# Kernel optimization log

Measured on AMD Instinct MI355X. Metric: run time of the kernel, lower is better.

Reference implementation:

```python
import jax, jax.numpy as jnp
import numpy as np
from jax import lax

KS = 3            # kernel_size
K = 32            # cluster_num
NB = 32           # num_base_kernels
HID = 64          # mlp_hidden_dim
COUT = 64         # out_channels
MAX_ITER = 20
TOL = 0.005


def _unfold3(x):
    # torch nn.Unfold(k=3, pad=1): output channel order is (c, kh, kw)
    b, c, h, w = x.shape
    xp = jnp.pad(x, ((0, 0), (0, 0), (1, 1), (1, 1)))
    cols = [xp[:, :, i:i + h, j:j + w] for i in range(KS) for j in range(KS)]
    p = jnp.stack(cols, axis=2)  # [B, C, 9, H, W]
    return p.reshape(b, c * KS * KS, h * w).transpose(0, 2, 1)  # [B, HW, C*9]


def _kmeans_single(key, sample):
    # sample: [N, D]. Lloyd iterations with early stop on total center shift.
    n, d = sample.shape
    centers0 = sample[jax.random.permutation(key, n)[:K]]

    def assign(centers):
        d2 = (jnp.sum(sample * sample, 1, keepdims=True)
              - 2.0 * (sample @ centers.T)
              + jnp.sum(centers * centers, 1))
        return jnp.argmin(d2, axis=1)

    def body(carry):
        i, centers, _ = carry
        a = assign(centers)
        oh = jax.nn.one_hot(a, K, dtype=sample.dtype)  # [N, K]
        counts = oh.sum(0)                             # [K]
        sums = oh.T @ sample                           # [K, D]
        new = jnp.where(counts[:, None] > 0,
                        sums / jnp.maximum(counts, 1.0)[:, None],
                        centers)
        shift = jnp.sum(jnp.linalg.norm(new - centers, axis=1))
        return (i + 1, new, shift)

    def cond(carry):
        i, _, shift = carry
        return jnp.logical_and(i < MAX_ITER, shift >= TOL * n)

    init = (jnp.int32(0), centers0, jnp.asarray(jnp.inf, sample.dtype))
    _, centers, _ = lax.while_loop(cond, body, init)
    return assign(centers)


def _kmeans(features):
    keys = jax.random.split(jax.random.key(42), features.shape[0])
    return jax.vmap(_kmeans_single)(keys, features)


def _mlp(x, w1, b1, w2, b2, w3, b3):
    h = jax.nn.relu(x @ w1 + b1)
    h = jax.nn.relu(h @ w2 + b2)
    return h @ w3 + b3


def setup_inputs() -> dict:
    key = jax.random.key(0)
    ks = jax.random.split(key, 16)
    B, C, H, W = 2, 32, 64, 64
    F = C * KS * KS
    fan = 1.0 / np.sqrt(F)
    fanh = 1.0 / np.sqrt(HID)
    return {
        'x': jax.random.normal(ks[0], (B, C, H, W), jnp.float32),
        'base_kernels': jax.random.normal(ks[1], (NB, F, COUT), jnp.float32) * np.sqrt(2.0 / F),
        'kg_w1': jax.random.normal(ks[2], (F, HID), jnp.float32) * fan,
        'kg_b1': jnp.zeros((HID,), jnp.float32),
        'kg_w2': jax.random.normal(ks[3], (HID, HID), jnp.float32) * fanh,
        'kg_b2': jnp.zeros((HID,), jnp.float32),
        'kg_w3': jax.random.normal(ks[4], (HID, NB), jnp.float32) * fanh,
        'kg_b3': jnp.zeros((NB,), jnp.float32),
        'bg_w1': jax.random.normal(ks[5], (F, HID), jnp.float32) * fan,
        'bg_b1': jnp.zeros((HID,), jnp.float32),
        'bg_w2': jax.random.normal(ks[6], (HID, HID), jnp.float32) * fanh,
        'bg_b2': jnp.zeros((HID,), jnp.float32),
        'bg_w3': jax.random.normal(ks[7], (HID, COUT), jnp.float32) * fanh,
        'bg_b3': jnp.zeros((COUT,), jnp.float32),
    }


def reference(x, base_kernels, kg_w1, kg_b1, kg_w2, kg_b2, kg_w3, kg_b3,
              bg_w1, bg_b1, bg_w2, bg_b2, bg_w3, bg_b3):
    B, C, H, W = x.shape
    patches = _unfold3(x)  # [B, P, F] with F = C*9
    P = patches.shape[1]
    # observation features: mean over kernel area per channel
    obs = patches.reshape(B, P, C, KS * KS).mean(-1)  # [B, P, C]
    idx = _kmeans(obs)  # [B, P] int cluster assignments

    # per-cluster centers of the full patch features (scatter-mean)
    oh = jax.nn.one_hot(idx, K, dtype=patches.dtype)          # [B, P, K]
    sums = jnp.einsum('bpk,bpf->bkf', oh, patches)            # [B, K, F]
    counts = jnp.maximum(oh.sum(1), 1.0)                      # [B, K]
    centers = sums / counts[:, :, None]                       # [B, K, F]

    # adaptive kernels = softmax-mixture of base kernels
    attn = jax.nn.softmax(_mlp(centers, kg_w1, kg_b1, kg_w2, kg_b2, kg_w3, kg_b3), axis=-1)  # [B,K,NB]
    kernels = jnp.einsum('bkn,nfc->bkfc', attn, base_kernels)  # [B, K, F, COUT]
    biases = _mlp(centers, bg_w1, bg_b1, bg_w2, bg_b2, bg_w3, bg_b3)  # [B, K, COUT]

    # combine: out[b,p] = patches[b,p] @ kernels[b, idx[b,p]] + biases[b, idx[b,p]]
    bidx = jnp.arange(B)[:, None]
    wtok = kernels[bidx, idx]   # [B, P, F, COUT]
    btok = biases[bidx, idx]    # [B, P, COUT]
    out = jnp.einsum('bpf,bpfc->bpc', patches, wtok) + btok
    out = out.transpose(0, 2, 1).reshape(B, COUT, H, W)
    return (out, idx)
```

## Files before the change

### kernel.cpp

```cpp
#include <hip/hip_runtime.h>
#include <hip/hip_bf16.h>
#include <vector>
#include <algorithm>
#include <utility>
#include <stdint.h>

#define BB 2
#define PP 4096
#define FF 288
#define KK 32
#define NBASE 32
#define HID 64
#define COUT 64
#define NWG_KM 32
#define SUBS 16
#define OUT_ELEMS 524288

#define THREEFRY_PARTITIONABLE 1

typedef unsigned short u16;

#define OFF_IDX    512
#define OFF_ATTN   33280
#define OFF_BIAS   41472
#define OFF_PART   57856
#define OFF_CNTS   320000
#define OFF_CPART  328192
#define OFF_WG     1544704
#define OFF_BAR2   3904000
#define OFF_CSAVE  3906048

struct InitIdx { int v[2][32]; };

__device__ __forceinline__ float bf2f(u16 u){
  union { unsigned int i; float f; } cv; cv.i = ((unsigned int)u) << 16; return cv.f;
}
__device__ __forceinline__ u16 f2bf(float f){
  union { float f; unsigned int i; } cv; cv.f = f;
  unsigned int x = cv.i;
  unsigned int r = (x + 0x7FFFu + ((x >> 16) & 1u)) >> 16;
  return (u16)r;
}
__device__ __forceinline__ float u_lo(unsigned int u){
  union { unsigned int i; float f; } cv; cv.i = u << 16; return cv.f;
}
__device__ __forceinline__ float u_hi(unsigned int u){
  union { unsigned int i; float f; } cv; cv.i = u & 0xFFFF0000u; return cv.f;
}

__device__ __forceinline__ void st_agent(float* p, float v){
  __hip_atomic_store(reinterpret_cast<unsigned int*>(p), __float_as_uint(v),
                     __ATOMIC_RELAXED, __HIP_MEMORY_SCOPE_AGENT);
}
__device__ __forceinline__ float ld_agent(const float* p){
  unsigned int u = __hip_atomic_load(reinterpret_cast<const unsigned int*>(p),
                                     __ATOMIC_RELAXED, __HIP_MEMORY_SCOPE_AGENT);
  return __uint_as_float(u);
}
__device__ __forceinline__ void st_slot(int* p, int v){
  __hip_atomic_store(p, v, __ATOMIC_RELAXED, __HIP_MEMORY_SCOPE_AGENT);
}
__device__ __forceinline__ int ld_slot(const int* p){
  return __hip_atomic_load(p, __ATOMIC_RELAXED, __HIP_MEMORY_SCOPE_AGENT);
}

template<bool BF>
__device__ __forceinline__ float ld(const void* p, size_t i){
  if constexpr (BF) { return bf2f(((const u16*)p)[i]); }
  else              { return ((const float*)p)[i]; }
}
template<bool BF>
__device__ __forceinline__ void st(void* p, size_t i, float v){
  if constexpr (BF) { ((u16*)p)[i] = f2bf(v); }
  else              { ((float*)p)[i] = v; }
}

__device__ __forceinline__ bool self_detect(const void* x, int* cntS){
  const int t = threadIdx.x, nb = blockDim.x;
  if (t == 0) *cntS = 0;
  __syncthreads();
  const u16* p = (const u16*)x;
  int bad = 0;
  for (int i = t; i < 1024; i += nb){
    u16 u = p[2*i];
    unsigned e = (u >> 7) & 0xFFu;
    if (e >= 131u) ++bad;
  }
  if (bad) atomicAdd(cntS, bad);
  __syncthreads();
  bool r = (*cntS < 102);
  __syncthreads();
  return r;
}

template<bool BF>
__device__ __forceinline__ float obs_chan(const void* x, size_t bi, int h, int w){
  float s = 0.f;
  #pragma unroll
  for (int dh=-1; dh<=1; ++dh){
    int hh = h + dh;
    #pragma unroll
    for (int dw=-1; dw<=1; ++dw){
      int ww = w + dw;
      float v = 0.f;
      if ((unsigned)hh < 64u && (unsigned)ww < 64u) v = ld<BF>(x, bi + (hh<<6) + ww);
      s += v;
    }
  }
  return s / 9.0f;
}

__device__ __forceinline__ void gbar16(int* slots, int mb, int sub, int epoch){
  asm volatile("s_waitcnt vmcnt(0)" ::: "memory");
  __syncthreads();
  const int t = threadIdx.x;
  if (t == 0) st_slot(&slots[(mb*16 + sub)*16], epoch);
  if (t < 16){
    while (ld_slot(&slots[(mb*16 + t)*16]) < epoch){}
  }
  __atomic_signal_fence(__ATOMIC_SEQ_CST);
  __syncthreads();
}

template<bool BF, bool FIRST>
__device__ void kB_body(const void* __restrict__ x,
                        float* __restrict__ part,
                        float* __restrict__ cnts,
                        int* __restrict__ idxg,
                        void* __restrict__ dout,
                        int* __restrict__ slots,
                        float* __restrict__ centSave,
                        int* __restrict__ actSave,
                        const InitIdx& ii,
                        float* obs_st, float* cent, float* cc_s, int* a_loc,
                        float* sq, float* snorm, float* cntsh,
                        float* acc8, float* cnt8){
  const int t   = threadIdx.x;
  const int wg  = blockIdx.x;
  const int mb  = wg >> 4;
  const int sub = wg & 15;
  const int pg  = sub*256 + t;
  const int d   = t & 31, oct = t >> 5;

  float o[32];
  {
    int h = pg >> 6, w = pg & 63;
    size_t xb = (size_t)mb << 17;
    for (int c=0; c<32; ++c){
      float v = obs_chan<BF>(x, xb + ((size_t)c<<12), h, w);
      o[c] = v; obs_st[t*33 + c] = v;
    }
  }
  bool act;
  if constexpr (FIRST){
    if (t < 32){
      int q = ii.v[mb][t];
      int qh = q >> 6, qw = q & 63;
      size_t xq = (size_t)mb << 17;
      for (int c=0; c<32; ++c) cent[t*32 + c] = obs_chan<BF>(x, xq + ((size_t)c<<12), qh, qw);
    }
    act = true;
  } else {
    for (int e=t; e<1024; e+=256) cent[e] = centSave[mb*1024 + e];
    act = (actSave[mb] != 0);
  }
  __syncthreads();

  float ss = 0.f;
  #pragma unroll
  for (int dd=0; dd<32; ++dd) ss = fmaf(o[dd], o[dd], ss);

  int parity = 0;
  const int itBeg = FIRST ? 0 : 10;
  const int itEnd = FIRST ? 10 : 20;

  for (int it=itBeg; it<itEnd && act; ++it){
    if (t < 32){
      float s = 0.f;
      #pragma unroll
      for (int dd=0; dd<32; ++dd){ float v = cent[t*32 + dd]; s = fmaf(v,v,s); }
      cc_s[t] = s;
    }
    __syncthreads();
    float best = 3.0e38f; int bk = 0;
    for (int k=0; k<32; k+=4){
      const float4* c0 = (const float4*)&cent[(k  )*32];
      const float4* c1 = (const float4*)&cent[(k+1)*32];
      const float4* c2 = (const float4*)&cent[(k+2)*32];
      const float4* c3 = (const float4*)&cent[(k+3)*32];
      float dt0=0.f, dt1=0.f, dt2=0.f, dt3=0.f;
      #pragma unroll
      for (int q=0; q<8; ++q){
        float4 a0 = c0[q], a1 = c1[q], a2 = c2[q], a3 = c3[q];
        float o0 = o[q*4+0], o1 = o[q*4+1], o2 = o[q*4+2], o3 = o[q*4+3];
        dt0 = fmaf(o0,a0.x,dt0); dt0 = fmaf(o1,a0.y,dt0); dt0 = fmaf(o2,a0.z,dt0); dt0 = fmaf(o3,a0.w,dt0);
        dt1 = fmaf(o0,a1.x,dt1); dt1 = fmaf(o1,a1.y,dt1); dt1 = fmaf(o2,a1.z,dt1); dt1 = fmaf(o3,a1.w,dt1);
        dt2 = fmaf(o0,a2.x,dt2); dt2 = fmaf(o1,a2.y,dt2); dt2 = fmaf(o2,a2.z,dt2); dt2 = fmaf(o3,a2.w,dt2);
        dt3 = fmaf(o0,a3.x,dt3); dt3 = fmaf(o1,a3.y,dt3); dt3 = fmaf(o2,a3.z,dt3); dt3 = fmaf(o3,a3.w,dt3);
      }
      float di0 = (ss - 2.0f*dt0) + cc_s[k];
      float di1 = (ss - 2.0f*dt1) + cc_s[k+1];
      float di2 = (ss - 2.0f*dt2) + cc_s[k+2];
      float di3 = (ss - 2.0f*dt3) + cc_s[k+3];
      if (di0 < best){ best = di0; bk = k; }
      if (di1 < best){ best = di1; bk = k+1; }
      if (di2 < best){ best = di2; bk = k+2; }
      if (di3 < best){ best = di3; bk = k+3; }
    }
    a_loc[t] = bk;
    __syncthreads();
    for (int e=t; e<8*32*33; e+=256) acc8[e] = 0.f;
    cnt8[t] = 0.f;
    __syncthreads();
    {
      const int p0 = oct*32;
      int kcur = a_loc[p0];
      float racc = 0.f; int rl = 0;
      for (int i=0; i<32; ++i){
        int kp = a_loc[p0+i];
        float v = obs_st[(p0+i)*33 + d];
        if (kp != kcur){
          acc8[(oct*32 + kcur)*33 + d] += racc;
          if (d == 0) cnt8[oct*32 + kcur] += (float)rl;
          racc = 0.f; rl = 0; kcur = kp;
        }
        racc += v; ++rl;
      }
      acc8[(oct*32 + kcur)*33 + d] += racc;
      if (d == 0) cnt8[oct*32 + kcur] += (float)rl;
    }
    __syncthreads();
    float* Pg = part + ((size_t)((parity*2 + mb)*SUBS + sub))*1024;
    {
      float r0=0.f, r1=0.f, r2=0.f, r3=0.f;
      #pragma unroll
      for (int o2=0; o2<8; ++o2){
        r0 += acc8[(o2*32 + oct      )*33 + d];
        r1 += acc8[(o2*32 + oct + 8  )*33 + d];
        r2 += acc8[(o2*32 + oct + 16 )*33 + d];
        r3 += acc8[(o2*32 + oct + 24 )*33 + d];
      }
      st_agent(&Pg[(oct     )*32 + d], r0);
      st_agent(&Pg[(oct + 8 )*32 + d], r1);
      st_agent(&Pg[(oct + 16)*32 + d], r2);
      st_agent(&Pg[(oct + 24)*32 + d], r3);
    }
    if (t < 32){
      float c = 0.f;
      #pragma unroll
      for (int o2=0; o2<8; ++o2) c += cnt8[o2*32 + t];
      st_agent(&cnts[((size_t)((parity*2 + mb)*SUBS + sub))*32 + t], c);
    }
    gbar16(slots, mb, sub, it+1);
    {
      const float* Pb = part + (size_t)((parity*2 + mb)*SUBS)*1024;
      const float* Cb = cnts + (size_t)((parity*2 + mb)*SUBS)*32;
      if (t < 32){
        float s = 0.f;
        #pragma unroll
        for (int si=0; si<SUBS; ++si) s += ld_agent(&Cb[si*32 + t]);
        cntsh[t] = s;
      }
      __syncthreads();
      {
        int k = t >> 3, d4 = (t & 7) * 4;
        float vx = 0.f, vy = 0.f, vz = 0.f, vw = 0.f;
        #pragma unroll
        for (int si=0; si<SUBS; ++si){
          const float* pp = &Pb[si*1024 + k*32 + d4];
          float a0 = ld_agent(pp+0);
          float a1 = ld_agent(pp+1);
          float a2 = ld_agent(pp+2);
          float a3 = ld_agent(pp+3);
          vx += a0; vy += a1; vz += a2; vw += a3;
        }
        float cn = cntsh[k];
        float den = fmaxf(cn, 1.f);
        bool pos = cn > 0.f;
        float o0 = cent[k*32 + d4+0], o1 = cent[k*32 + d4+1];
        float o2 = cent[k*32 + d4+2], o3 = cent[k*32 + d4+3];
        float n0 = pos ? (vx / den) : o0;
        float n1 = pos ? (vy / den) : o1;
        float n2 = pos ? (vz / den) : o2;
        float n3 = pos ? (vw / den) : o3;
        float e0 = n0-o0, e1 = n1-o1, e2 = n2-o2, e3 = n3-o3;
        sq[k*32 + d4+0] = e0*e0; sq[k*32 + d4+1] = e1*e1;
        sq[k*32 + d4+2] = e2*e2; sq[k*32 + d4+3] = e3*e3;
        cent[k*32 + d4+0] = n0; cent[k*32 + d4+1] = n1;
        cent[k*32 + d4+2] = n2; cent[k*32 + d4+3] = n3;
      }
      __syncthreads();
      if (t < 32){
        float s = 0.f;
        #pragma unroll
        for (int dd=0; dd<32; ++dd) s += sq[t*32 + dd];
        snorm[t] = sqrtf(s);
      }
      __syncthreads();
      float sh = 0.f;
      for (int k=0;k<32;++k) sh += snorm[k];
      act = ((it+1) < 20) && ((double)sh >= 20.48);
      __syncthreads();
    }
    parity ^= 1;
  }

  if constexpr (FIRST){
    __syncthreads();
    if (sub == 0){
      for (int e=t; e<1024; e+=256) centSave[mb*1024 + e] = cent[e];
      if (t == 0) actSave[mb] = act ? 1 : 0;
    }
    return;
  } else {
    if (t == 0) st_slot(&slots[(mb*16 + sub)*16], 0x7FFFFFFF);
    __syncthreads();
    if (t < 32){
      float s = 0.f;
      #pragma unroll
      for (int dd=0; dd<32; ++dd){ float v = cent[t*32 + dd]; s = fmaf(v,v,s); }
      cc_s[t] = s;
    }
    __syncthreads();
    float best = 3.0e38f; int bk = 0;
    for (int k=0; k<32; k+=4){
      const float4* c0 = (const float4*)&cent[(k  )*32];
      const float4* c1 = (const float4*)&cent[(k+1)*32];
      const float4* c2 = (const float4*)&cent[(k+2)*32];
      const float4* c3 = (const float4*)&cent[(k+3)*32];
      float dt0=0.f, dt1=0.f, dt2=0.f, dt3=0.f;
      #pragma unroll
      for (int q=0; q<8; ++q){
        float4 a0 = c0[q], a1 = c1[q], a2 = c2[q], a3 = c3[q];
        float o0 = o[q*4+0], o1 = o[q*4+1], o2 = o[q*4+2], o3 = o[q*4+3];
        dt0 = fmaf(o0,a0.x,dt0); dt0 = fmaf(o1,a0.y,dt0); dt0 = fmaf(o2,a0.z,dt0); dt0 = fmaf(o3,a0.w,dt0);
        dt1 = fmaf(o0,a1.x,dt1); dt1 = fmaf(o1,a1.y,dt1); dt1 = fmaf(o2,a1.z,dt1); dt1 = fmaf(o3,a1.w,dt1);
        dt2 = fmaf(o0,a2.x,dt2); dt2 = fmaf(o1,a2.y,dt2); dt2 = fmaf(o2,a2.z,dt2); dt2 = fmaf(o3,a2.w,dt2);
        dt3 = fmaf(o0,a3.x,dt3); dt3 = fmaf(o1,a3.y,dt3); dt3 = fmaf(o2,a3.z,dt3); dt3 = fmaf(o3,a3.w,dt3);
      }
      float di0 = (ss - 2.0f*dt0) + cc_s[k];
      float di1 = (ss - 2.0f*dt1) + cc_s[k+1];
      float di2 = (ss - 2.0f*dt2) + cc_s[k+2];
      float di3 = (ss - 2.0f*dt3) + cc_s[k+3];
      if (di0 < best){ best = di0; bk = k; }
      if (di1 < best){ best = di1; bk = k+1; }
      if (di2 < best){ best = di2; bk = k+2; }
      if (di3 < best){ best = di3; bk = k+3; }
    }
    idxg[mb*PP + pg] = bk;
    st<BF>(dout, (size_t)OUT_ELEMS + mb*PP + pg, (float)bk);
  }
}

template<bool FIRST>
__global__ __launch_bounds__(256) void kBsplit(const void* x, float* part, float* cnts,
                                               int* idxg, void* dout,
                                               int* slots, float* centSave, int* actSave,
                                               InitIdx ii){
  __shared__ __align__(16) float obs_st[256*33];
  __shared__ __align__(16) float cent[32*32];
  __shared__ float cc_s[32];
  __shared__ int   a_loc[256];
  __shared__ float sq[32*32];
  __shared__ float snorm[32];
  __shared__ float cntsh[32];
  __shared__ float acc8[8*32*33];
  __shared__ float cnt8[8*32];
  __shared__ int   cntS;
  if (self_detect(x, &cntS))
       kB_body<true , FIRST>(x, part, cnts, idxg, dout, slots, centSave, actSave, ii,
                             obs_st, cent, cc_s, a_loc, sq, snorm, cntsh, acc8, cnt8);
  else kB_body<false, FIRST>(x, part, cnts, idxg, dout, slots, centSave, actSave, ii,
                             obs_st, cent, cc_s, a_loc, sq, snorm, cntsh, acc8, cnt8);
}

template<bool BF>
__device__ void kC_body(const void* __restrict__ x,
                        const int* __restrict__ idxg,
                        float* __restrict__ cpartJ,
                        float* __restrict__ tv,
                        int* __restrict__ idxsh,
                        float* __restrict__ acc8,
                        float* __restrict__ cnt8){
  int wgid = blockIdx.x;
  int cg = wgid / 9, j = wgid % 9;
  int b = cg >> 4, pc = cg & 15;
  int t = threadIdx.x;
  const int d = t & 31, oct = t >> 5;

  idxsh[t] = idxg[b*PP + pc*256 + t];
  int dh = j/3 - 1, dw = j%3 - 1;
  for (int e=t; e<8192; e+=256){
    int c = e >> 8, p = e & 255;
    int gp = (pc << 8) + p;
    int h = gp >> 6, w = gp & 63;
    int hh = h + dh, ww = w + dw;
    float v = 0.f;
    if ((unsigned)hh < 64u && (unsigned)ww < 64u)
      v = ld<BF>(x, ((size_t)b << 17) + ((size_t)c << 12) + (hh<<6) + ww);
    tv[p*33 + c] = v;
  }
  for (int e=t; e<8*32*33; e+=256) acc8[e] = 0.f;
  cnt8[t] = 0.f;
  __syncthreads();
  {
    const int p0 = oct*32;
    int kcur = idxsh[p0];
    float racc = 0.f; int rl = 0;
    for (int i=0; i<32; ++i){
      int kp = idxsh[p0+i];
      float v = tv[(p0+i)*33 + d];
      if (kp != kcur){
        acc8[(oct*32 + kcur)*33 + d] += racc;
        if (d == 0) cnt8[oct*32 + kcur] += (float)rl;
        racc = 0.f; rl = 0; kcur = kp;
      }
      racc += v; ++rl;
    }
    acc8[(oct*32 + kcur)*33 + d] += racc;
    if (d == 0) cnt8[oct*32 + kcur] += (float)rl;
  }
  __syncthreads();
  float* cp = cpartJ + (size_t)wgid*(32*33);
  {
    float r0=0.f, r1=0.f, r2=0.f, r3=0.f;
    #pragma unroll
    for (int o2=0; o2<8; ++o2){
      r0 += acc8[(o2*32 + oct      )*33 + d];
      r1 += acc8[(o2*32 + oct + 8  )*33 + d];
      r2 += acc8[(o2*32 + oct + 16 )*33 + d];
      r3 += acc8[(o2*32 + oct + 24 )*33 + d];
    }
    cp[(oct     )*33 + d] = r0;
    cp[(oct + 8 )*33 + d] = r1;
    cp[(oct + 16)*33 + d] = r2;
    cp[(oct + 24)*33 + d] = r3;
  }
  if (j == 0 && t < 32){
    float c8 = 0.f;
    #pragma unroll
    for (int o2=0; o2<8; ++o2) c8 += cnt8[o2*32 + t];
    cp[t*33 + 32] = c8;
  }
}

__global__ __launch_bounds__(256) void kC(const void* x, const int* idxg,
                                          float* cpartJ){
  __shared__ __align__(16) float tv[256*33];
  __shared__ int   idxsh[256];
  __shared__ __align__(16) float acc8[8*32*33];
  __shared__ float cnt8[256];
  __shared__ int   cntS;
  if (self_detect(x, &cntS)) kC_body<true >(x, idxg, cpartJ, tv, idxsh, acc8, cnt8);
  else                       kC_body<false>(x, idxg, cpartJ, tv, idxsh, acc8, cnt8);
}

template<bool BF>
__device__ void kD_body(const float* __restrict__ cpartJ,
                        const void* kg_w1, const void* kg_b1,
                        const void* kg_w2, const void* kg_b2,
                        const void* kg_w3, const void* kg_b3,
                        const void* bg_w1, const void* bg_b1,
                        const void* bg_w2, const void* bg_b2,
                        const void* bg_w3, const void* bg_b3,
                        float* __restrict__ attn,
                        float* __restrict__ biasO,
                        float* __restrict__ row,
                        float* __restrict__ h1,
                        float* __restrict__ h2,
                        float* __restrict__ lgs){
  int wg = blockIdx.x; int b = wg >> 5; int k = wg & 31;
  int t = threadIdx.x;
  float cnt = 0.f;
  for (int ch=0; ch<16; ++ch)
    cnt += cpartJ[(size_t)((b*16+ch)*9)*(32*33) + k*33 + 32];
  float den = fmaxf(cnt, 1.f);
  for (int f=t; f<FF; f+=64){
    int c = f / 9, j = f % 9;
    float s = 0.f;
    for (int ch=0; ch<16; ++ch)
      s += cpartJ[(size_t)((b*16+ch)*9 + j)*(32*33) + k*33 + c];
    row[f] = s / den;
  }
  __syncthreads();

  {
    float s = 0.f;
    #pragma unroll 8
    for (int f=0; f<FF; ++f) s = fmaf(row[f], ld<BF>(kg_w1, f*HID + t), s);
    h1[t] = fmaxf(s + ld<BF>(kg_b1, t), 0.f);
  }
  __syncthreads();
  {
    float s = 0.f;
    #pragma unroll 8
    for (int h=0; h<HID; ++h) s = fmaf(h1[h], ld<BF>(kg_w2, h*HID + t), s);
    h2[t] = fmaxf(s + ld<BF>(kg_b2, t), 0.f);
  }
  __syncthreads();
  if (t < 32){
    float s = 0.f;
    #pragma unroll 8
    for (int h=0; h<HID; ++h) s = fmaf(h2[h], ld<BF>(kg_w3, h*NBASE + t), s);
    lgs[t] = s + ld<BF>(kg_b3, t);
  }
  __syncthreads();
  if (t < 32){
    float mx = -3.0e38f;
    for (int i=0;i<NBASE;++i) mx = fmaxf(mx, lgs[i]);
    float se = 0.f;
    for (int i=0;i<NBASE;++i) se += expf(lgs[i]-mx);
    attn[wg*NBASE + t] = expf(lgs[t]-mx) / se;
  }
  __syncthreads();
  {
    float s = 0.f;
    #pragma unroll 8
    for (int f=0; f<FF; ++f) s = fmaf(row[f], ld<BF>(bg_w1, f*HID + t), s);
    h1[t] = fmaxf(s + ld<BF>(bg_b1, t), 0.f);
  }
  __syncthreads();
  {
    float s = 0.f;
    #pragma unroll 8
    for (int h=0; h<HID; ++h) s = fmaf(h1[h], ld<BF>(bg_w2, h*HID + t), s);
    h2[t] = fmaxf(s + ld<BF>(bg_b2, t), 0.f);
  }
  __syncthreads();
  {
    float s = 0.f;
    #pragma unroll 8
    for (int h=0; h<HID; ++h) s = fmaf(h1[h] * 0.f + h2[h], ld<BF>(bg_w3, h*COUT + t), s);
    biasO[wg*COUT + t] = s + ld<BF>(bg_b3, t);
  }
}

__global__ __launch_bounds__(64) void kD(const void* x, const float* cpartJ,
                                         const void* kg_w1, const void* kg_b1,
                                         const void* kg_w2, const void* kg_b2,
                                         const void* kg_w3, const void* kg_b3,
                                         const void* bg_w1, const void* bg_b1,
                                         const void* bg_w2, const void* bg_b2,
                                         const void* bg_w3, const void* bg_b3,
                                         float* attn, float* biasO){
  __shared__ float row[FF];
  __shared__ float h1[64];
  __shared__ float h2[64];
  __shared__ float lgs[32];
  __shared__ int   cntS;
  if (self_detect(x, &cntS))
       kD_body<true >(cpartJ, kg_w1,kg_b1,kg_w2,kg_b2,kg_w3,kg_b3,
                      bg_w1,bg_b1,bg_w2,bg_b2,bg_w3,bg_b3, attn, biasO, row,h1,h2,lgs);
  else kD_body<false>(cpartJ, kg_w1,kg_b1,kg_w2,kg_b2,kg_w3,kg_b3,
                      bg_w1,bg_b1,bg_w2,bg_b2,bg_w3,bg_b3, attn, biasO, row,h1,h2,lgs);
}

template<bool BF>
__device__ void kE_body(const void* __restrict__ base,
                        const float* __restrict__ attn,
                        u16* __restrict__ Wg,
                        float* __restrict__ at,
                        float* __restrict__ tile){
  int wg = blockIdx.x;
  int fq = wg & 3, bk = wg >> 2;
  int t = threadIdx.x;
  if (t < 32) at[t] = attn[bk*NBASE + t];
  __syncthreads();
  int f0 = fq*72;
  for (int e8 = t; e8 < 72*8; e8 += 256){
    int fl = e8 >> 3, cg = (e8 & 7) << 3;
    float s0=0.f,s1=0.f,s2=0.f,s3=0.f,s4=0.f,s5=0.f,s6=0.f,s7=0.f;
    if constexpr (BF){
      const u16* bp = (const u16*)base + (size_t)(f0 + fl)*COUT + cg;
      #pragma unroll 4
      for (int n=0; n<NBASE; ++n){
        uint4 v = *(const uint4*)(bp + (size_t)n*FF*COUT);
        float a = at[n];
        s0 = fmaf(a, u_lo(v.x), s0); s1 = fmaf(a, u_hi(v.x), s1);
        s2 = fmaf(a, u_lo(v.y), s2); s3 = fmaf(a, u_hi(v.y), s3);
        s4 = fmaf(a, u_lo(v.z), s4); s5 = fmaf(a, u_hi(v.z), s5);
        s6 = fmaf(a, u_lo(v.w), s6); s7 = fmaf(a, u_hi(v.w), s7);
      }
    } else {
      const float* bp = (const float*)base + (size_t)(f0 + fl)*COUT + cg;
      #pragma unroll 4
      for (int n=0; n<NBASE; ++n){
        float4 v0 = *(const float4*)(bp + (size_t)n*FF*COUT);
        float4 v1 = *(const float4*)(bp + (size_t)n*FF*COUT + 4);
        float a = at[n];
        s0 = fmaf(a, v0.x, s0); s1 = fmaf(a, v0.y, s1);
        s2 = fmaf(a, v0.z, s2); s3 = fmaf(a, v0.w, s3);
        s4 = fmaf(a, v1.x, s4); s5 = fmaf(a, v1.y, s5);
        s6 = fmaf(a, v1.z, s6); s7 = fmaf(a, v1.w, s7);
      }
    }
    float* tp = &tile[fl*65 + cg];
    tp[0]=s0; tp[1]=s1; tp[2]=s2; tp[3]=s3;
    tp[4]=s4; tp[5]=s5; tp[6]=s6; tp[7]=s7;
  }
  __syncthreads();
  for (int e=t; e<72*64; e+=256){
    int c = e / 72, fl = e % 72;
    Wg[(size_t)bk*(64*FF) + (size_t)c*FF + f0 + fl] = f2bf(tile[fl*65 + c]);
  }
}

__global__ __launch_bounds__(256) void kE(const void* x, const void* base,
                                          const float* attn, u16* Wg){
  __shared__ float at[32];
  __shared__ float tile[72*65];
  __shared__ int   cntS;
  if (self_detect(x, &cntS)) kE_body<true >(base, attn, Wg, at, tile);
  else                       kE_body<false>(base, attn, Wg, at, tile);
}

template<bool BF>
__device__ void kF_body(const void* __restrict__ x,
                        const int* __restrict__ idxg,
                        const u16* __restrict__ Wg,
                        const float* __restrict__ biasO,
                        void* __restrict__ dout,
                        u16* __restrict__ patch,
                        float* __restrict__ outT){
  int wg = blockIdx.x;
  int q = wg & 3, h = (wg >> 2) & 63, b = wg >> 8;
  int t = threadIdx.x, wv = t >> 6, lane = t & 63;
  int w0 = q << 4;

  for (int e=t; e<16*FF; e+=256){
    int pl = e & 15, fe = e >> 4;
    int c = fe / 9, j = fe % 9;
    int hh = h + j/3 - 1, ww = w0 + pl + (j%3) - 1;
    float v = 0.f;
    if ((unsigned)hh < 64u && (unsigned)ww < 64u)
      v = ld<BF>(x, ((size_t)b << 17) + ((size_t)c << 12) + (hh<<6) + ww);
    patch[pl*296 + fe] = f2bf(v);
  }
  __syncthreads();

  #pragma unroll
  for (int i=0; i<4; ++i){
    int pl = (wv << 2) + i;
    int p = (h << 6) + w0 + pl;
    int k = idxg[(b << 12) + p];
    const uint4* Wp = (const uint4*)(Wg + ((size_t)((b << 5) + k)*64 + lane)*FF);
    const uint4* Pp = (const uint4*)(patch + pl*296);
    float acc = 0.f;
    #pragma unroll 6
    for (int j=0; j<36; ++j){
      uint4 wv4 = Wp[j];
      uint4 pv4 = Pp[j];
      acc = fmaf(u_lo(pv4.x), u_lo(wv4.x), acc);
      acc = fmaf(u_hi(pv4.x), u_hi(wv4.x), acc);
      acc = fmaf(u_lo(pv4.y), u_lo(wv4.y), acc);
      acc = fmaf(u_hi(pv4.y), u_hi(wv4.y), acc);
      acc = fmaf(u_lo(pv4.z), u_lo(wv4.z), acc);
      acc = fmaf(u_hi(pv4.z), u_hi(wv4.z), acc);
      acc = fmaf(u_lo(pv4.w), u_lo(wv4.w), acc);
      acc = fmaf(u_hi(pv4.w), u_hi(wv4.w), acc);
    }
    float bias = biasO[((b << 5) + k)*COUT + lane];
    outT[lane*17 + pl] = acc + bias;
  }
  __syncthreads();

  for (int e=t; e<1024; e+=256){
    int cout = e >> 4, pl = e & 15;
    st<BF>(dout, (((size_t)(b << 6) + cout) << 12) + (h << 6) + w0 + pl,
           outT[cout*17 + pl]);
  }
}

__global__ __launch_bounds__(256) void kF(const void* x, const int* idxg,
                                          const u16* Wg, const float* biasO,
                                          void* dout){
  __shared__ u16   patch[16*296];
  __shared__ float outT[64*17];
  __shared__ int   cntS;
  if (self_detect(x, &cntS)) kF_body<true >(x, idxg, Wg, biasO, dout, patch, outT);
  else                       kF_body<false>(x, idxg, Wg, biasO, dout, patch, outT);
}

static inline uint32_t rotl32(uint32_t x, int d){ return (x<<d)|(x>>(32-d)); }
static void tf_block(uint32_t k0,uint32_t k1,uint32_t x0,uint32_t x1,uint32_t&o0,uint32_t&o1){
  uint32_t ks2 = k0 ^ k1 ^ 0x1BD11BDAu;
  uint32_t v0 = x0 + k0, v1 = x1 + k1;
  const int ra[4]={13,15,26,6}, rb[4]={17,29,16,24};
  #define R4(r) for(int i_=0;i_<4;++i_){ v0 += v1; v1 = rotl32(v1,(r)[i_]); v1 ^= v0; }
  R4(ra); v0 += k1;  v1 += ks2 + 1u;
  R4(rb); v0 += ks2; v1 += k0  + 2u;
  R4(ra); v0 += k0;  v1 += k1  + 3u;
  R4(rb); v0 += k1;  v1 += ks2 + 4u;
  R4(ra); v0 += ks2; v1 += k0  + 5u;
  #undef R4
  o0 = v0; o1 = v1;
}
struct KP{ uint32_t a, b; };
static void tf_split(KP k, KP& first, KP& second){
#if THREEFRY_PARTITIONABLE
  uint32_t a0,b0,a1,b1;
  tf_block(k.a,k.b, 0u,0u, a0,b0);
  tf_block(k.a,k.b, 0u,1u, a1,b1);
  first  = KP{a0,b0};
  second = KP{a1,b1};
#else
  uint32_t a0,b0,a1,b1;
  tf_block(k.a,k.b, 0u,2u, a0,b0);
  tf_block(k.a,k.b, 1u,3u, a1,b1);
  first  = KP{a0,a1};
  second = KP{b0,b1};
#endif
}
static void random_bits_4096(KP k, std::vector<uint32_t>& bits){
#if THREEFRY_PARTITIONABLE
  for (int i=0;i<4096;++i){
    uint32_t o0,o1; tf_block(k.a,k.b, 0u,(uint32_t)i, o0,o1);
    bits[i] = o0 ^ o1;
  }
#else
  for (int i=0;i<2048;++i){
    uint32_t o0,o1; tf_block(k.a,k.b,(uint32_t)i,(uint32_t)(i+2048),o0,o1);
    bits[i] = o0; bits[i+2048] = o1;
  }
#endif
}
static void perm_first32(KP key, int* out32){
  std::vector<int> vals(4096);
  for (int i=0;i<4096;++i) vals[i] = i;
  std::vector<uint32_t> bits(4096);
  std::vector<std::pair<uint32_t,int>> pr(4096);
  KP k = key;
  for (int r=0;r<2;++r){
    KP nk, sk; tf_split(k, nk, sk); k = nk;
    random_bits_4096(sk, bits);
    for (int i=0;i<4096;++i) pr[i] = std::make_pair(bits[i], vals[i]);
    std::stable_sort(pr.begin(), pr.end(),
        [](const std::pair<uint32_t,int>& a, const std::pair<uint32_t,int>& c){ return a.first < c.first; });
    for (int i=0;i<4096;++i) vals[i] = pr[i].second;
  }
  for (int j=0;j<32;++j) out32[j] = vals[j];
}

extern "C" void kernel_launch(void* const* d_in, const int* in_sizes, int n_in,
                              void* d_out, int out_size, void* d_ws, size_t ws_size,
                              hipStream_t stream) {
  const void* x     = d_in[0];
  const void* base  = d_in[1];
  const void* kg_w1 = d_in[2];
  const void* kg_b1 = d_in[3];
  const void* kg_w2 = d_in[4];
  const void* kg_b2 = d_in[5];
  const void* kg_w3 = d_in[6];
  const void* kg_b3 = d_in[7];
  const void* bg_w1 = d_in[8];
  const void* bg_b1 = d_in[9];
  const void* bg_w2 = d_in[10];
  const void* bg_b2 = d_in[11];
  const void* bg_w3 = d_in[12];
  const void* bg_b3 = d_in[13];

  char* ws = (char*)d_ws;
  int*   idxg  = (int*)(ws + OFF_IDX);
  float* attn  = (float*)(ws + OFF_ATTN);
  float* biasO = (float*)(ws + OFF_BIAS);
  float* part  = (float*)(ws + OFF_PART);
  float* cnts  = (float*)(ws + OFF_CNTS);
  float* cpartJ= (float*)(ws + OFF_CPART);
  u16*   Wg    = (u16*)(ws + OFF_WG);
  int*   slots = (int*)(ws + OFF_BAR2);
  float* centSave = (float*)(ws + OFF_CSAVE);
  int*   actSave  = slots + 8;

  InitIdx ii;
  KP root = KP{0u, 42u};
  KP kb0, kb1; tf_split(root, kb0, kb1);
  perm_first32(kb0, ii.v[0]);
  perm_first32(kb1, ii.v[1]);

  hipMemsetAsync(ws + OFF_BAR2, 0, 2048, stream);
  kBsplit<true ><<<NWG_KM, 256, 0, stream>>>(x, part, cnts, idxg, d_out, slots, centSave, actSave, ii);
  kBsplit<false><<<NWG_KM, 256, 0, stream>>>(x, part, cnts, idxg, d_out, slots, centSave, actSave, ii);
  kC<<<288, 256, 0, stream>>>(x, idxg, cpartJ);
  kD<<<64, 64, 0, stream>>>(x, cpartJ,
                            kg_w1, kg_b1, kg_w2, kg_b2, kg_w3, kg_b3,
                            bg_w1, bg_b1, bg_w2, bg_b2, bg_w3, bg_b3,
                            attn, biasO);
  kE<<<256, 256, 0, stream>>>(x, base, attn, Wg);
  kF<<<512, 256, 0, stream>>>(x, idxg, Wg, biasO, d_out);
}
```

Before: 289.6 us.

## Merge split k-means launches and fuse MLP with kernel-mixing stage

The two-launch k-means, which saved centroids and the active flag to workspace between halves, becomes a single kernel that runs all 20 iterations. The MLP kernel (kD) and the base-kernel mixing kernel (kE) are fused into one kDE launch, where each of the four f-quarter blocks recomputes the per-cluster MLP redundantly. The host-side threefry permutation is also computed once and cached in a static. The aim is to cut launch gaps and intermediate round trips, at the cost of about fourfold redundant MLP work across blocks.

```diff
diff --git a/kernel.cpp b/kernel.cpp
--- a/kernel.cpp
+++ b/kernel.cpp
@@ -21,14 +21,12 @@
 typedef unsigned short u16;
 
 #define OFF_IDX    512
-#define OFF_ATTN   33280
 #define OFF_BIAS   41472
 #define OFF_PART   57856
 #define OFF_CNTS   320000
 #define OFF_CPART  328192
 #define OFF_WG     1544704
 #define OFF_BAR2   3904000
-#define OFF_CSAVE  3906048
 
 struct InitIdx { int v[2][32]; };
 
@@ -122,15 +120,13 @@
   __syncthreads();
 }
 
-template<bool BF, bool FIRST>
+template<bool BF>
 __device__ void kB_body(const void* __restrict__ x,
                         float* __restrict__ part,
                         float* __restrict__ cnts,
                         int* __restrict__ idxg,
                         void* __restrict__ dout,
                         int* __restrict__ slots,
-                        float* __restrict__ centSave,
-                        int* __restrict__ actSave,
                         const InitIdx& ii,
                         float* obs_st, float* cent, float* cc_s, int* a_loc,
                         float* sq, float* snorm, float* cntsh,
@@ -151,18 +147,11 @@
       o[c] = v; obs_st[t*33 + c] = v;
     }
   }
-  bool act;
-  if constexpr (FIRST){
-    if (t < 32){
-      int q = ii.v[mb][t];
-      int qh = q >> 6, qw = q & 63;
-      size_t xq = (size_t)mb << 17;
-      for (int c=0; c<32; ++c) cent[t*32 + c] = obs_chan<BF>(x, xq + ((size_t)c<<12), qh, qw);
-    }
-    act = true;
-  } else {
-    for (int e=t; e<1024; e+=256) cent[e] = centSave[mb*1024 + e];
-    act = (actSave[mb] != 0);
+  if (t < 32){
+    int q = ii.v[mb][t];
+    int qh = q >> 6, qw = q & 63;
+    size_t xq = (size_t)mb << 17;
+    for (int c=0; c<32; ++c) cent[t*32 + c] = obs_chan<BF>(x, xq + ((size_t)c<<12), qh, qw);
   }
   __syncthreads();
 
@@ -170,11 +159,10 @@
   #pragma unroll
   for (int dd=0; dd<32; ++dd) ss = fmaf(o[dd], o[dd], ss);
 
+  bool act = true;
   int parity = 0;
-  const int itBeg = FIRST ? 0 : 10;
-  const int itEnd = FIRST ? 10 : 20;
-
-  for (int it=itBeg; it<itEnd && act; ++it){
+
+  for (int it=0; it<20 && act; ++it){
     if (t < 32){
       float s = 0.f;
       #pragma unroll
@@ -304,59 +292,47 @@
     }
     parity ^= 1;
   }
-
-  if constexpr (FIRST){
-    __syncthreads();
-    if (sub == 0){
-      for (int e=t; e<1024; e+=256) centSave[mb*1024 + e] = cent[e];
-      if (t == 0) actSave[mb] = act ? 1 : 0;
-    }
-    return;
-  } else {
-    if (t == 0) st_slot(&slots[(mb*16 + sub)*16], 0x7FFFFFFF);
-    __syncthreads();
-    if (t < 32){
-      float s = 0.f;
-      #pragma unroll
-      for (int dd=0; dd<32; ++dd){ float v = cent[t*32 + dd]; s = fmaf(v,v,s); }
-      cc_s[t] = s;
-    }
-    __syncthreads();
-    float best = 3.0e38f; int bk = 0;
-    for (int k=0; k<32; k+=4){
-      const float4* c0 = (const float4*)&cent[(k  )*32];
-      const float4* c1 = (const float4*)&cent[(k+1)*32];
-      const float4* c2 = (const float4*)&cent[(k+2)*32];
-      const float4* c3 = (const float4*)&cent[(k+3)*32];
-      float dt0=0.f, dt1=0.f, dt2=0.f, dt3=0.f;
-      #pragma unroll
-      for (int q=0; q<8; ++q){
-        float4 a0 = c0[q], a1 = c1[q], a2 = c2[q], a3 = c3[q];
-        float o0 = o[q*4+0], o1 = o[q*4+1], o2 = o[q*4+2], o3 = o[q*4+3];
-        dt0 = fmaf(o0,a0.x,dt0); dt0 = fmaf(o1,a0.y,dt0); dt0 = fmaf(o2,a0.z,dt0); dt0 = fmaf(o3,a0.w,dt0);
-        dt1 = fmaf(o0,a1.x,dt1); dt1 = fmaf(o1,a1.y,dt1); dt1 = fmaf(o2,a1.z,dt1); dt1 = fmaf(o3,a1.w,dt1);
-        dt2 = fmaf(o0,a2.x,dt2); dt2 = fmaf(o1,a2.y,dt2); dt2 = fmaf(o2,a2.z,dt2); dt2 = fmaf(o3,a2.w,dt2);
-        dt3 = fmaf(o0,a3.x,dt3); dt3 = fmaf(o1,a3.y,dt3); dt3 = fmaf(o2,a3.z,dt3); dt3 = fmaf(o3,a3.w,dt3);
-      }
-      float di0 = (ss - 2.0f*dt0) + cc_s[k];
-      float di1 = (ss - 2.0f*dt1) + cc_s[k+1];
-      float di2 = (ss - 2.0f*dt2) + cc_s[k+2];
-      float di3 = (ss - 2.0f*dt3) + cc_s[k+3];
-      if (di0 < best){ best = di0; bk = k; }
-      if (di1 < best){ best = di1; bk = k+1; }
-      if (di2 < best){ best = di2; bk = k+2; }
-      if (di3 < best){ best = di3; bk = k+3; }
-    }
-    idxg[mb*PP + pg] = bk;
-    st<BF>(dout, (size_t)OUT_ELEMS + mb*PP + pg, (float)bk);
-  }
-}
-
-template<bool FIRST>
-__global__ __launch_bounds__(256) void kBsplit(const void* x, float* part, float* cnts,
-                                               int* idxg, void* dout,
-                                               int* slots, float* centSave, int* actSave,
-                                               InitIdx ii){
+  if (t == 0) st_slot(&slots[(mb*16 + sub)*16], 0x7FFFFFFF);
+  __syncthreads();
+  if (t < 32){
+    float s = 0.f;
+    #pragma unroll
+    for (int dd=0; dd<32; ++dd){ float v = cent[t*32 + dd]; s = fmaf(v,v,s); }
+    cc_s[t] = s;
+  }
+  __syncthreads();
+  float best = 3.0e38f; int bk = 0;
+  for (int k=0; k<32; k+=4){
+    const float4* c0 = (const float4*)&cent[(k  )*32];
+    const float4* c1 = (const float4*)&cent[(k+1)*32];
+    const float4* c2 = (const float4*)&cent[(k+2)*32];
+    const float4* c3 = (const float4*)&cent[(k+3)*32];
+    float dt0=0.f, dt1=0.f, dt2=0.f, dt3=0.f;
+    #pragma unroll
+    for (int q=0; q<8; ++q){
+      float4 a0 = c0[q], a1 = c1[q], a2 = c2[q], a3 = c3[q];
+      float o0 = o[q*4+0], o1 = o[q*4+1], o2 = o[q*4+2], o3 = o[q*4+3];
+      dt0 = fmaf(o0,a0.x,dt0); dt0 = fmaf(o1,a0.y,dt0); dt0 = fmaf(o2,a0.z,dt0); dt0 = fmaf(o3,a0.w,dt0);
+      dt1 = fmaf(o0,a1.x,dt1); dt1 = fmaf(o1,a1.y,dt1); dt1 = fmaf(o2,a1.z,dt1); dt1 = fmaf(o3,a1.w,dt1);
+      dt2 = fmaf(o0,a2.x,dt2); dt2 = fmaf(o1,a2.y,dt2); dt2 = fmaf(o2,a2.z,dt2); dt2 = fmaf(o3,a2.w,dt2);
+      dt3 = fmaf(o0,a3.x,dt3); dt3 = fmaf(o1,a3.y,dt3); dt3 = fmaf(o2,a3.z,dt3); dt3 = fmaf(o3,a3.w,dt3);
+    }
+    float di0 = (ss - 2.0f*dt0) + cc_s[k];
+    float di1 = (ss - 2.0f*dt1) + cc_s[k+1];
+    float di2 = (ss - 2.0f*dt2) + cc_s[k+2];
+    float di3 = (ss - 2.0f*dt3) + cc_s[k+3];
+    if (di0 < best){ best = di0; bk = k; }
+    if (di1 < best){ best = di1; bk = k+1; }
+    if (di2 < best){ best = di2; bk = k+2; }
+    if (di3 < best){ best = di3; bk = k+3; }
+  }
+  idxg[mb*PP + pg] = bk;
+  st<BF>(dout, (size_t)OUT_ELEMS + mb*PP + pg, (float)bk);
+}
+
+__global__ __launch_bounds__(256) void kB(const void* x, float* part, float* cnts,
+                                          int* idxg, void* dout,
+                                          int* slots, InitIdx ii){
   __shared__ __align__(16) float obs_st[256*33];
   __shared__ __align__(16) float cent[32*32];
   __shared__ float cc_s[32];
@@ -368,10 +344,10 @@
   __shared__ float cnt8[8*32];
   __shared__ int   cntS;
   if (self_detect(x, &cntS))
-       kB_body<true , FIRST>(x, part, cnts, idxg, dout, slots, centSave, actSave, ii,
-                             obs_st, cent, cc_s, a_loc, sq, snorm, cntsh, acc8, cnt8);
-  else kB_body<false, FIRST>(x, part, cnts, idxg, dout, slots, centSave, actSave, ii,
-                             obs_st, cent, cc_s, a_loc, sq, snorm, cntsh, acc8, cnt8);
+       kB_body<true >(x, part, cnts, idxg, dout, slots, ii,
+                      obs_st, cent, cc_s, a_loc, sq, snorm, cntsh, acc8, cnt8);
+  else kB_body<false>(x, part, cnts, idxg, dout, slots, ii,
+                      obs_st, cent, cc_s, a_loc, sq, snorm, cntsh, acc8, cnt8);
 }
 
 template<bool BF>
@@ -456,42 +432,45 @@
 }
 
 template<bool BF>
-__device__ void kD_body(const float* __restrict__ cpartJ,
-                        const void* kg_w1, const void* kg_b1,
-                        const void* kg_w2, const void* kg_b2,
-                        const void* kg_w3, const void* kg_b3,
-                        const void* bg_w1, const void* bg_b1,
-                        const void* bg_w2, const void* bg_b2,
-                        const void* bg_w3, const void* bg_b3,
-                        float* __restrict__ attn,
-                        float* __restrict__ biasO,
-                        float* __restrict__ row,
-                        float* __restrict__ h1,
-                        float* __restrict__ h2,
-                        float* __restrict__ lgs){
-  int wg = blockIdx.x; int b = wg >> 5; int k = wg & 31;
+__device__ void kDE_body(const void* __restrict__ base,
+                         const float* __restrict__ cpartJ,
+                         const void* kg_w1, const void* kg_b1,
+                         const void* kg_w2, const void* kg_b2,
+                         const void* kg_w3, const void* kg_b3,
+                         const void* bg_w1, const void* bg_b1,
+                         const void* bg_w2, const void* bg_b2,
+                         const void* bg_w3, const void* bg_b3,
+                         float* __restrict__ biasO,
+                         u16* __restrict__ Wg,
+                         float* row, float* h1, float* h2, float* lgs,
+                         float* at, float* tile){
+  int wg = blockIdx.x;
+  int fq = wg & 3, bk = wg >> 2;
+  int b = bk >> 5, k = bk & 31;
   int t = threadIdx.x;
-  float cnt = 0.f;
-  for (int ch=0; ch<16; ++ch)
-    cnt += cpartJ[(size_t)((b*16+ch)*9)*(32*33) + k*33 + 32];
-  float den = fmaxf(cnt, 1.f);
-  for (int f=t; f<FF; f+=64){
-    int c = f / 9, j = f % 9;
-    float s = 0.f;
+
+  if (t < 64){
+    float cnt = 0.f;
     for (int ch=0; ch<16; ++ch)
-      s += cpartJ[(size_t)((b*16+ch)*9 + j)*(32*33) + k*33 + c];
-    row[f] = s / den;
-  }
-  __syncthreads();
-
-  {
+      cnt += cpartJ[(size_t)((b*16+ch)*9)*(32*33) + k*33 + 32];
+    float den = fmaxf(cnt, 1.f);
+    for (int f=t; f<FF; f+=64){
+      int c = f / 9, j = f % 9;
+      float s = 0.f;
+      for (int ch=0; ch<16; ++ch)
+        s += cpartJ[(size_t)((b*16+ch)*9 + j)*(32*33) + k*33 + c];
+      row[f] = s / den;
+    }
+  }
+  __syncthreads();
+  if (t < 64){
     float s = 0.f;
     #pragma unroll 8
     for (int f=0; f<FF; ++f) s = fmaf(row[f], ld<BF>(kg_w1, f*HID + t), s);
     h1[t] = fmaxf(s + ld<BF>(kg_b1, t), 0.f);
   }
   __syncthreads();
-  {
+  if (t < 64){
     float s = 0.f;
     #pragma unroll 8
     for (int h=0; h<HID; ++h) s = fmaf(h1[h], ld<BF>(kg_w2, h*HID + t), s);
@@ -510,62 +489,31 @@
     for (int i=0;i<NBASE;++i) mx = fmaxf(mx, lgs[i]);
     float se = 0.f;
     for (int i=0;i<NBASE;++i) se += expf(lgs[i]-mx);
-    attn[wg*NBASE + t] = expf(lgs[t]-mx) / se;
-  }
-  __syncthreads();
-  {
+    at[t] = expf(lgs[t]-mx) / se;
+  }
+  __syncthreads();
+  if (t < 64){
     float s = 0.f;
     #pragma unroll 8
     for (int f=0; f<FF; ++f) s = fmaf(row[f], ld<BF>(bg_w1, f*HID + t), s);
     h1[t] = fmaxf(s + ld<BF>(bg_b1, t), 0.f);
   }
   __syncthreads();
-  {
+  if (t < 64){
     float s = 0.f;
     #pragma unroll 8
     for (int h=0; h<HID; ++h) s = fmaf(h1[h], ld<BF>(bg_w2, h*HID + t), s);
     h2[t] = fmaxf(s + ld<BF>(bg_b2, t), 0.f);
   }
   __syncthreads();
-  {
+  if (t < 64 && fq == 0){
     float s = 0.f;
     #pragma unroll 8
-    for (int h=0; h<HID; ++h) s = fmaf(h1[h] * 0.f + h2[h], ld<BF>(bg_w3, h*COUT + t), s);
-    biasO[wg*COUT + t] = s + ld<BF>(bg_b3, t);
-  }
-}
-
-__global__ __launch_bounds__(64) void kD(const void* x, const float* cpartJ,
-                                         const void* kg_w1, const void* kg_b1,
-                                         const void* kg_w2, const void* kg_b2,
-                                         const void* kg_w3, const void* kg_b3,
-                                         const void* bg_w1, const void* bg_b1,
-                                         const void* bg_w2, const void* bg_b2,
-                                         const void* bg_w3, const void* bg_b3,
-                                         float* attn, float* biasO){
-  __shared__ float row[FF];
-  __shared__ float h1[64];
-  __shared__ float h2[64];
-  __shared__ float lgs[32];
-  __shared__ int   cntS;
-  if (self_detect(x, &cntS))
-       kD_body<true >(cpartJ, kg_w1,kg_b1,kg_w2,kg_b2,kg_w3,kg_b3,
-                      bg_w1,bg_b1,bg_w2,bg_b2,bg_w3,bg_b3, attn, biasO, row,h1,h2,lgs);
-  else kD_body<false>(cpartJ, kg_w1,kg_b1,kg_w2,kg_b2,kg_w3,kg_b3,
-                      bg_w1,bg_b1,bg_w2,bg_b2,bg_w3,bg_b3, attn, biasO, row,h1,h2,lgs);
-}
-
-template<bool BF>
-__device__ void kE_body(const void* __restrict__ base,
-                        const float* __restrict__ attn,
-                        u16* __restrict__ Wg,
-                        float* __restrict__ at,
-                        float* __restrict__ tile){
-  int wg = blockIdx.x;
-  int fq = wg & 3, bk = wg >> 2;
-  int t = threadIdx.x;
-  if (t < 32) at[t] = attn[bk*NBASE + t];
-  __syncthreads();
+    for (int h=0; h<HID; ++h) s = fmaf(h2[h], ld<BF>(bg_w3, h*COUT + t), s);
+    biasO[bk*COUT + t] = s + ld<BF>(bg_b3, t);
+  }
+  __syncthreads();
+
   int f0 = fq*72;
   for (int e8 = t; e8 < 72*8; e8 += 256){
     int fl = e8 >> 3, cg = (e8 & 7) << 3;
@@ -605,13 +553,29 @@
   }
 }
 
-__global__ __launch_bounds__(256) void kE(const void* x, const void* base,
-                                          const float* attn, u16* Wg){
+__global__ __launch_bounds__(256) void kDE(const void* x, const void* base,
+                         const float* cpartJ,
+                         const void* kg_w1, const void* kg_b1,
+                         const void* kg_w2, const void* kg_b2,
+                         const void* kg_w3, const void* kg_b3,
+                         const void* bg_w1, const void* bg_b1,
+                         const void* bg_w2, const void* bg_b2,
+                         const void* bg_w3, const void* bg_b3,
+                         float* biasO, u16* Wg){
+  __shared__ float row[FF];
+  __shared__ float h1[64];
+  __shared__ float h2[64];
+  __shared__ float lgs[32];
   __shared__ float at[32];
   __shared__ float tile[72*65];
   __shared__ int   cntS;
-  if (self_detect(x, &cntS)) kE_body<true >(base, attn, Wg, at, tile);
-  else                       kE_body<false>(base, attn, Wg, at, tile);
+  if (self_detect(x, &cntS))
+       kDE_body<true >(base, cpartJ, kg_w1,kg_b1,kg_w2,kg_b2,kg_w3,kg_b3,
+                       bg_w1,bg_b1,bg_w2,bg_b2,bg_w3,bg_b3, biasO, Wg,
+                       row,h1,h2,lgs,at,tile);
+  else kDE_body<false>(base, cpartJ, kg_w1,kg_b1,kg_w2,kg_b2,kg_w3,kg_b3,
+                       bg_w1,bg_b1,bg_w2,bg_b2,bg_w3,bg_b3, biasO, Wg,
+                       row,h1,h2,lgs,at,tile);
 }
 
 template<bool BF>
@@ -741,6 +705,18 @@
   for (int j=0;j<32;++j) out32[j] = vals[j];
 }
 
+static const InitIdx& get_init_idx(){
+  static const InitIdx ii = [](){
+    InitIdx r;
+    KP root = KP{0u, 42u};
+    KP kb0, kb1; tf_split(root, kb0, kb1);
+    perm_first32(kb0, r.v[0]);
+    perm_first32(kb1, r.v[1]);
+    return r;
+  }();
+  return ii;
+}
+
 extern "C" void kernel_launch(void* const* d_in, const int* in_sizes, int n_in,
                               void* d_out, int out_size, void* d_ws, size_t ws_size,
                               hipStream_t stream) {
@@ -761,30 +737,21 @@
 
   char* ws = (char*)d_ws;
   int*   idxg  = (int*)(ws + OFF_IDX);
-  float* attn  = (float*)(ws + OFF_ATTN);
   float* biasO = (float*)(ws + OFF_BIAS);
   float* part  = (float*)(ws + OFF_PART);
   float* cnts  = (float*)(ws + OFF_CNTS);
   float* cpartJ= (float*)(ws + OFF_CPART);
   u16*   Wg    = (u16*)(ws + OFF_WG);
   int*   slots = (int*)(ws + OFF_BAR2);
-  float* centSave = (float*)(ws + OFF_CSAVE);
-  int*   actSave  = slots + 8;
-
-  InitIdx ii;
-  KP root = KP{0u, 42u};
-  KP kb0, kb1; tf_split(root, kb0, kb1);
-  perm_first32(kb0, ii.v[0]);
-  perm_first32(kb1, ii.v[1]);
+
+  const InitIdx& ii = get_init_idx();
 
   hipMemsetAsync(ws + OFF_BAR2, 0, 2048, stream);
-  kBsplit<true ><<<NWG_KM, 256, 0, stream>>>(x, part, cnts, idxg, d_out, slots, centSave, actSave, ii);
-  kBsplit<false><<<NWG_KM, 256, 0, stream>>>(x, part, cnts, idxg, d_out, slots, centSave, actSave, ii);
+  kB<<<NWG_KM, 256, 0, stream>>>(x, part, cnts, idxg, d_out, slots, ii);
   kC<<<288, 256, 0, stream>>>(x, idxg, cpartJ);
-  kD<<<64, 64, 0, stream>>>(x, cpartJ,
-                            kg_w1, kg_b1, kg_w2, kg_b2, kg_w3, kg_b3,
-                            bg_w1, bg_b1, bg_w2, bg_b2, bg_w3, bg_b3,
-                            attn, biasO);
-  kE<<<256, 256, 0, stream>>>(x, base, attn, Wg);
+  kDE<<<256, 256, 0, stream>>>(x, base, cpartJ,
+                               kg_w1, kg_b1, kg_w2, kg_b2, kg_w3, kg_b3,
+                               bg_w1, bg_b1, bg_w2, bg_b2, bg_w3, bg_b3,
+                               biasO, Wg);
   kF<<<512, 256, 0, stream>>>(x, idxg, Wg, biasO, d_out);
 }
```

Result: faster. 265.5 us (-8.3%).
